# Kernel tuning notes

Measured on AMD Instinct MI355X. Metric: run time of the kernel, lower is better.

Reference implementation:

```python
import jax, jax.numpy as jnp
import numpy as np

N_NODES = 100_000
N_EDGES = 3_200_000
N_FEAT = 128
N_HID = 8
N_CLASSES = 10


def setup_inputs() -> dict:
    key = jax.random.key(0)
    ks = jax.random.split(key, 16)
    g = lambda k, shape, fan_in: jax.random.normal(k, shape, jnp.float32) / np.sqrt(fan_in)
    inp = {}
    inp['x'] = jax.random.normal(ks[0], (N_NODES, N_FEAT), jnp.float32)
    inp['edge_index'] = jax.random.randint(ks[1], (2, N_EDGES), 0, N_NODES, jnp.int32)
    # lin: Linear(F, 8)
    inp['lin_w'] = g(ks[2], (N_FEAT, N_HID), N_FEAT)
    inp['lin_b'] = jnp.zeros((N_HID,), jnp.float32)
    # conv1: GATConv(8, 8, heads=2)
    inp['w1'] = g(ks[3], (N_HID, 2 * N_HID), N_HID)
    inp['a1_src'] = g(ks[4], (2, N_HID), N_HID)
    inp['a1_dst'] = g(ks[5], (2, N_HID), N_HID)
    inp['b1'] = jnp.zeros((2 * N_HID,), jnp.float32)
    # conv2: GATConv(16, 8, heads=2)
    inp['w2'] = g(ks[6], (2 * N_HID, 2 * N_HID), 2 * N_HID)
    inp['a2_src'] = g(ks[7], (2, N_HID), N_HID)
    inp['a2_dst'] = g(ks[8], (2, N_HID), N_HID)
    inp['b2'] = jnp.zeros((2 * N_HID,), jnp.float32)
    # conv3: GATConv(16, num_classes, heads=1, concat=False)
    inp['w3'] = g(ks[9], (2 * N_HID, N_CLASSES), 2 * N_HID)
    inp['a3_src'] = g(ks[10], (1, N_CLASSES), N_CLASSES)
    inp['a3_dst'] = g(ks[11], (1, N_CLASSES), N_CLASSES)
    inp['b3'] = jnp.zeros((N_CLASSES,), jnp.float32)
    return inp


def _gat_conv(x, W, a_src, a_dst, b, src, dst, heads, out_c, concat):
    """PyG GATConv with pre-appended self-loops in (src, dst)."""
    N = x.shape[0]
    xl = (x @ W).reshape(N, heads, out_c)                 # [N,H,C]
    alpha_src = (xl * a_src[None]).sum(-1)                # [N,H]
    alpha_dst = (xl * a_dst[None]).sum(-1)                # [N,H]
    e = jax.nn.leaky_relu(alpha_src[src] + alpha_dst[dst], 0.2)  # [E,H]
    # segment softmax over destination nodes
    m = jax.ops.segment_max(e, dst, num_segments=N)
    e = jnp.exp(e - m[dst])
    s = jax.ops.segment_sum(e, dst, num_segments=N)
    alpha = e / s[dst]                                    # [E,H]
    msg = xl[src] * alpha[:, :, None]                     # [E,H,C]
    out = jax.ops.segment_sum(msg, dst, num_segments=N)   # [N,H,C]
    out = out.reshape(N, heads * out_c) if concat else out.mean(axis=1)
    return out + b


def reference(x, edge_index, lin_w, lin_b, w1, a1_src, a1_dst, b1,
              w2, a2_src, a2_dst, b2, w3, a3_src, a3_dst, b3):
    N = x.shape[0]
    loops = jnp.arange(N, dtype=edge_index.dtype)
    src = jnp.concatenate([edge_index[0], loops])
    dst = jnp.concatenate([edge_index[1], loops])
    lrelu = lambda v: jax.nn.leaky_relu(v, 0.01)
    h = lrelu(x @ lin_w + lin_b)
    h = lrelu(_gat_conv(h, w1, a1_src, a1_dst, b1, src, dst, 2, N_HID, True))
    h = lrelu(_gat_conv(h, w2, a2_src, a2_dst, b2, src, dst, 2, N_HID, True))
    h = _gat_conv(h, w3, a3_src, a3_dst, b3, src, dst, 1, N_CLASSES, False)
    return jax.nn.log_softmax(h, axis=-1)
```

## Files before the change

### kernel.cpp

```cpp
#include <hip/hip_runtime.h>
#include <hip/hip_fp16.h>
#include <math.h>

#define N_NODES 100000
#define N_EDGES 3200000
#define ET (N_EDGES + N_NODES)
#define SLOT 80
#define KMAX 5
#define SHIFT 8
#define BNODES 256
#define NBUCK 391
#define BCAP 9088
#define P1_T 1024
#define E_PER 16
#define P1_WG ((N_EDGES + P1_T * E_PER - 1) / (P1_T * E_PER))
#define SCAN_T 1024
#define SCAN_CHUNK 98
#define LOG2E 1.44269504088896f

__device__ __forceinline__ float lrelu(float v, float s) { return v > 0.f ? v : v * s; }
__device__ __forceinline__ float fexp2(float x) { return __builtin_amdgcn_exp2f(x); }

template <int CTRL>
__device__ __forceinline__ float dppmov(float v) {
    return __int_as_float(__builtin_amdgcn_update_dpp(0, __float_as_int(v), CTRL, 0xF, 0xF, true));
}

__device__ __forceinline__ void reduce16(float& v, float& ssum, float pa0, float pa1,
                                         float pa2, float pa3, int lane) {
    int b0 = lane & 1, b1 = (lane >> 1) & 1;
    float k0 = b0 ? pa2 : pa0, g0 = b0 ? pa0 : pa2;
    float k1 = b0 ? pa3 : pa1, g1 = b0 ? pa1 : pa3;
    float q0 = k0 + dppmov<0xB1>(g0);
    float q1 = k1 + dppmov<0xB1>(g1);
    float kk = b1 ? q1 : q0, gg = b1 ? q0 : q1;
    v = kk + dppmov<0x4E>(gg);
    v += __shfl_xor(v, 4, 64);
    v += __shfl_xor(v, 8, 64);
    ssum += dppmov<0xB1>(ssum);
    ssum += dppmov<0x4E>(ssum);
    ssum += __shfl_xor(ssum, 4, 64);
    ssum += __shfl_xor(ssum, 8, 64);
}

__global__ void __launch_bounds__(P1_T) part_kernel(const int* __restrict__ ei,
                                                    int* __restrict__ bcur,
                                                    unsigned* __restrict__ pairs) {
    __shared__ int hist[NBUCK];
    __shared__ int gbase[NBUCK];
    int t = threadIdx.x;
    for (int i = t; i < NBUCK; i += P1_T) hist[i] = 0;
    __syncthreads();
    int base = blockIdx.x * (P1_T * E_PER);
    int s[E_PER], d[E_PER], r[E_PER];
#pragma unroll
    for (int k = 0; k < E_PER; k++) {
        int e = base + k * P1_T + t;
        if (e < N_EDGES) {
            s[k] = ei[e];
            d[k] = ei[N_EDGES + e];
            r[k] = atomicAdd(&hist[d[k] >> SHIFT], 1);
        }
    }
    __syncthreads();
    for (int i = t; i < NBUCK; i += P1_T)
        gbase[i] = (hist[i] > 0) ? atomicAdd(&bcur[i], hist[i]) : 0;
    __syncthreads();
#pragma unroll
    for (int k = 0; k < E_PER; k++) {
        int e = base + k * P1_T + t;
        if (e < N_EDGES) {
            int b = d[k] >> SHIFT;
            int pos = gbase[b] + r[k];
            if (pos < BCAP)
                pairs[(size_t)b * BCAP + pos] =
                    ((unsigned)(d[k] & (BNODES - 1)) << 17) | (unsigned)s[k];
        }
    }
}

__global__ void build_kernel(const int* __restrict__ bcur, const unsigned* __restrict__ pairs,
                             int* __restrict__ csr, int* __restrict__ deg) {
    __shared__ int offs[BNODES];
    int b = blockIdx.x;
    int t = threadIdx.x;
    int node0 = b << SHIFT;
    int n = node0 + t;
    if (n < N_NODES) {
        csr[n * SLOT] = n;
        offs[t] = 1;
    } else offs[t] = 0;
    __syncthreads();
    int cnt = min(bcur[b], BCAP);
    for (int i = t; i < cnt; i += BNODES) {
        unsigned v = pairs[(size_t)b * BCAP + i];
        int ln = v >> 17;
        int s = v & 0x1FFFF;
        int pos = atomicAdd(&offs[ln], 1);
        if (pos < SLOT) csr[(node0 + ln) * SLOT + pos] = s;
    }
    __syncthreads();
    if (n < N_NODES) deg[n] = offs[t];
}

__global__ void count_kernel(const int* __restrict__ ei, int* __restrict__ deg) {
    int e = blockIdx.x * blockDim.x + threadIdx.x;
    if (e >= ET) return;
    int d = (e < N_EDGES) ? ei[N_EDGES + e] : (e - N_EDGES);
    atomicAdd(&deg[d], 1);
}

__global__ void scan_kernel(const int* __restrict__ deg, int* __restrict__ rowptr,
                            int* __restrict__ cursor) {
    __shared__ int sums[SCAN_T];
    int t = threadIdx.x;
    int start = t * SCAN_CHUNK;
    int end = min(start + SCAN_CHUNK, N_NODES);
    int s = 0;
    for (int i = start; i < end; i++) s += deg[i];
    sums[t] = s;
    __syncthreads();
    for (int off = 1; off < SCAN_T; off <<= 1) {
        int v = sums[t];
        int add = (t >= off) ? sums[t - off] : 0;
        __syncthreads();
        sums[t] = v + add;
        __syncthreads();
    }
    int base = (t > 0) ? sums[t - 1] : 0;
    for (int i = start; i < end; i++) {
        rowptr[i] = base;
        cursor[i] = base;
        base += deg[i];
    }
    if (t == SCAN_T - 1) rowptr[N_NODES] = base;
}

__global__ void scatter_kernel(const int* __restrict__ ei, int* __restrict__ cursor,
                               int* __restrict__ csr) {
    int e = blockIdx.x * blockDim.x + threadIdx.x;
    if (e >= ET) return;
    int s, d;
    if (e < N_EDGES) { s = ei[e]; d = ei[N_EDGES + e]; } else { s = d = e - N_EDGES; }
    int pos = atomicAdd(&cursor[d], 1);
    csr[pos] = s;
}

template <int CIN, int H, int C, int XLS>
__global__ void prep_kernel(const float* __restrict__ hin, const float* __restrict__ W,
                            const float* __restrict__ a_src, const float* __restrict__ a_dst,
                            __half* __restrict__ xl, float* __restrict__ asrc,
                            float* __restrict__ adst) {
    __shared__ float Ws[CIN * H * C];
    __shared__ float As[H * C];
    __shared__ float Ad[H * C];
    for (int i = threadIdx.x; i < CIN * H * C; i += blockDim.x) Ws[i] = W[i];
    for (int i = threadIdx.x; i < H * C; i += blockDim.x) {
        As[i] = a_src[i] * LOG2E;
        Ad[i] = a_dst[i] * LOG2E;
    }
    __syncthreads();
    int n = blockIdx.x * blockDim.x + threadIdx.x;
    if (n >= N_NODES) return;
    float hreg[CIN];
#pragma unroll
    for (int i = 0; i < CIN; i += 4) {
        float4 v = *(const float4*)&hin[n * CIN + i];
        hreg[i] = v.x; hreg[i + 1] = v.y; hreg[i + 2] = v.z; hreg[i + 3] = v.w;
    }
#pragma unroll
    for (int h = 0; h < H; h++) {
        float as = 0.f, ad = 0.f;
#pragma unroll
        for (int c = 0; c < C; c++) {
            float v = 0.f;
#pragma unroll
            for (int i = 0; i < CIN; i++) v += hreg[i] * Ws[i * H * C + h * C + c];
            xl[n * XLS + h * C + c] = __float2half_rn(v);
            as += v * As[h * C + c];
            ad += v * Ad[h * C + c];
        }
        asrc[n * H + h] = as;
        adst[n * H + h] = ad;
    }
#pragma unroll
    for (int c = H * C; c < XLS; c++) xl[n * XLS + c] = __float2half_rn(0.f);
}

template <int H, int C, int XLS>
__global__ __launch_bounds__(256) void prep_lin_kernel(
        const float* __restrict__ x, const float* __restrict__ lw, const float* __restrict__ lb,
        const float* __restrict__ W, const float* __restrict__ a_src,
        const float* __restrict__ a_dst, __half* __restrict__ xl,
        float* __restrict__ asrc, float* __restrict__ adst) {
    __shared__ float LW[128 * 8];
    __shared__ float Ws[8 * H * C];
    __shared__ float As[H * C];
    __shared__ float Ad[H * C];
    __shared__ float Lb[8];
    for (int i = threadIdx.x; i < 128 * 8; i += 256) LW[i] = lw[i];
    for (int i = threadIdx.x; i < 8 * H * C; i += 256) Ws[i] = W[i];
    for (int i = threadIdx.x; i < H * C; i += 256) {
        As[i] = a_src[i] * LOG2E;
        Ad[i] = a_dst[i] * LOG2E;
    }
    if (threadIdx.x < 8) Lb[threadIdx.x] = lb[threadIdx.x];
    __syncthreads();
    int n = blockIdx.x * blockDim.x + threadIdx.x;
    if (n >= N_NODES) return;
    float hreg[8];
#pragma unroll
    for (int c = 0; c < 8; c++) hreg[c] = 0.f;
#pragma unroll 8
    for (int i = 0; i < 128; i += 4) {
        float4 v = *(const float4*)&x[n * 128 + i];
#pragma unroll
        for (int c = 0; c < 8; c++) hreg[c] += v.x * LW[(i + 0) * 8 + c];
#pragma unroll
        for (int c = 0; c < 8; c++) hreg[c] += v.y * LW[(i + 1) * 8 + c];
#pragma unroll
        for (int c = 0; c < 8; c++) hreg[c] += v.z * LW[(i + 2) * 8 + c];
#pragma unroll
        for (int c = 0; c < 8; c++) hreg[c] += v.w * LW[(i + 3) * 8 + c];
    }
#pragma unroll
    for (int c = 0; c < 8; c++) hreg[c] = lrelu(hreg[c] + Lb[c], 0.01f);
#pragma unroll
    for (int h = 0; h < H; h++) {
        float as = 0.f, ad = 0.f;
#pragma unroll
        for (int c = 0; c < C; c++) {
            float v = 0.f;
#pragma unroll
            for (int i = 0; i < 8; i++) v += hreg[i] * Ws[i * H * C + h * C + c];
            xl[n * XLS + h * C + c] = __float2half_rn(v);
            as += v * As[h * C + c];
            ad += v * Ad[h * C + c];
        }
        asrc[n * H + h] = as;
        adst[n * H + h] = ad;
    }
#pragma unroll
    for (int c = H * C; c < XLS; c++) xl[n * XLS + c] = __float2half_rn(0.f);
}

__global__ __launch_bounds__(256) void gat64_h2(const int* __restrict__ cnt_,
                                                const int* __restrict__ csr,
                                                const float* __restrict__ asrc,
                                                const float* __restrict__ adst,
                                                const __half* __restrict__ xl,
                                                const float* __restrict__ b,
                                                float* __restrict__ hout) {
    int wg = blockIdx.x * 4 + (threadIdx.x >> 6);
    int lane = threadIdx.x & 63;
    int eg = lane & 15;
    int cp = lane >> 4;
    int h = cp >> 1;
    int n0 = wg * 2, n1 = n0 + 1;
    int cnt0 = min(cnt_[n0], SLOT);
    int cnt1 = min(cnt_[n1], SLOT);
    int ka0 = __builtin_amdgcn_readfirstlane((cnt0 + 15) >> 4);
    int ka1 = __builtin_amdgcn_readfirstlane((cnt1 + 15) >> 4);
    float ad0 = adst[n0 * 2 + h];
    float ad1 = adst[n1 * 2 + h];
    int idx0[KMAX], idx1[KMAX];
#pragma unroll
    for (int k = 0; k < KMAX; k++) {
        if (k < ka0) idx0[k] = csr[n0 * SLOT + eg + (k << 4)];
        if (k < ka1) idx1[k] = csr[n1 * SLOT + eg + (k << 4)];
    }
    float s0 = 0.f, a00 = 0.f, a01 = 0.f, a02 = 0.f, a03 = 0.f;
    float s1 = 0.f, a10 = 0.f, a11 = 0.f, a12 = 0.f, a13 = 0.f;
#pragma unroll
    for (int k = 0; k < KMAX; k++) {
        if (k < ka0) {
            bool vld = eg + (k << 4) < cnt0;
            int s = vld ? idx0[k] : 0;
            float av = asrc[s * 2 + h];
            float2 raw = *(const float2*)&xl[s * 16 + 4 * cp];
            float e = av + ad0;
            float w = fexp2(fmaxf(e, 0.2f * e));
            w = vld ? w : 0.f;
            float2 f01 = __half22float2(*(__half2*)&raw.x);
            float2 f23 = __half22float2(*(__half2*)&raw.y);
            s0 += w;
            a00 += w * f01.x; a01 += w * f01.y; a02 += w * f23.x; a03 += w * f23.y;
        }
        if (k < ka1) {
            bool vld = eg + (k << 4) < cnt1;
            int t = vld ? idx1[k] : 0;
            float av = asrc[t * 2 + h];
            float2 raw = *(const float2*)&xl[t * 16 + 4 * cp];
            float e = av + ad1;
            float w = fexp2(fmaxf(e, 0.2f * e));
            w = vld ? w : 0.f;
            float2 f01 = __half22float2(*(__half2*)&raw.x);
            float2 f23 = __half22float2(*(__half2*)&raw.y);
            s1 += w;
            a10 += w * f01.x; a11 += w * f01.y; a12 += w * f23.x; a13 += w * f23.y;
        }
    }
    float v0, v1;
    reduce16(v0, s0, a00, a01, a02, a03, lane);
    reduce16(v1, s1, a10, a11, a12, a13, lane);
    if ((lane & 12) == 0) {
        int ch = 4 * cp + 2 * (lane & 1) + ((lane >> 1) & 1);
        float bc = b[ch];
        hout[n0 * 16 + ch] = lrelu(v0 / s0 + bc, 0.01f);
        hout[n1 * 16 + ch] = lrelu(v1 / s1 + bc, 0.01f);
    }
}

__global__ __launch_bounds__(256) void gat64_ls(const int* __restrict__ cnt_,
                                                const int* __restrict__ csr,
                                                const float* __restrict__ asrc,
                                                const float* __restrict__ adst,
                                                const __half* __restrict__ xl,
                                                const float* __restrict__ b,
                                                float* __restrict__ out) {
    int wg = blockIdx.x * 4 + (threadIdx.x >> 6);
    int lane = threadIdx.x & 63;
    int eg = lane & 15;
    int cp = lane >> 4;
    int n0 = wg * 2, n1 = n0 + 1;
    int cnt0 = min(cnt_[n0], SLOT);
    int cnt1 = min(cnt_[n1], SLOT);
    int ka0 = __builtin_amdgcn_readfirstlane((cnt0 + 15) >> 4);
    int ka1 = __builtin_amdgcn_readfirstlane((cnt1 + 15) >> 4);
    float ad0 = adst[n0];
    float ad1 = adst[n1];
    int idx0[KMAX], idx1[KMAX];
#pragma unroll
    for (int k = 0; k < KMAX; k++) {
        if (k < ka0) idx0[k] = csr[n0 * SLOT + eg + (k << 4)];
        if (k < ka1) idx1[k] = csr[n1 * SLOT + eg + (k << 4)];
    }
    float s0 = 0.f, a00 = 0.f, a01 = 0.f, a02 = 0.f, a03 = 0.f;
    float s1 = 0.f, a10 = 0.f, a11 = 0.f, a12 = 0.f, a13 = 0.f;
#pragma unroll
    for (int k = 0; k < KMAX; k++) {
        if (k < ka0) {
            bool vld = eg + (k << 4) < cnt0;
            int s = vld ? idx0[k] : 0;
            float av = asrc[s];
            float2 raw = *(const float2*)&xl[s * 16 + 4 * cp];
            float e = av + ad0;
            float w = fexp2(fmaxf(e, 0.2f * e));
            w = vld ? w : 0.f;
            float2 f01 = __half22float2(*(__half2*)&raw.x);
            float2 f23 = __half22float2(*(__half2*)&raw.y);
            s0 += w;
            a00 += w * f01.x; a01 += w * f01.y; a02 += w * f23.x; a03 += w * f23.y;
        }
        if (k < ka1) {
            bool vld = eg + (k << 4) < cnt1;
            int t = vld ? idx1[k] : 0;
            float av = asrc[t];
            float2 raw = *(const float2*)&xl[t * 16 + 4 * cp];
            float e = av + ad1;
            float w = fexp2(fmaxf(e, 0.2f * e));
            w = vld ? w : 0.f;
            float2 f01 = __half22float2(*(__half2*)&raw.x);
            float2 f23 = __half22float2(*(__half2*)&raw.y);
            s1 += w;
            a10 += w * f01.x; a11 += w * f01.y; a12 += w * f23.x; a13 += w * f23.y;
        }
    }
    float v0, v1;
    reduce16(v0, s0, a00, a01, a02, a03, lane);
    reduce16(v1, s1, a10, a11, a12, a13, lane);
    int ch = 4 * cp + 2 * (lane & 1) + ((lane >> 1) & 1);
    float bc = (ch < 10) ? b[ch] : 0.f;
    float u0 = (ch < 10) ? v0 / s0 + bc : -INFINITY;
    float u1 = (ch < 10) ? v1 / s1 + bc : -INFINITY;
    float m0 = u0, m1 = u1;
    m0 = fmaxf(m0, dppmov<0xB1>(m0)); m1 = fmaxf(m1, dppmov<0xB1>(m1));
    m0 = fmaxf(m0, dppmov<0x4E>(m0)); m1 = fmaxf(m1, dppmov<0x4E>(m1));
    m0 = fmaxf(m0, __shfl_xor(m0, 16, 64)); m1 = fmaxf(m1, __shfl_xor(m1, 16, 64));
    m0 = fmaxf(m0, __shfl_xor(m0, 32, 64)); m1 = fmaxf(m1, __shfl_xor(m1, 32, 64));
    float e0 = (ch < 10) ? __expf(u0 - m0) : 0.f;
    float e1 = (ch < 10) ? __expf(u1 - m1) : 0.f;
    e0 += dppmov<0xB1>(e0); e1 += dppmov<0xB1>(e1);
    e0 += dppmov<0x4E>(e0); e1 += dppmov<0x4E>(e1);
    e0 += __shfl_xor(e0, 16, 64); e1 += __shfl_xor(e1, 16, 64);
    e0 += __shfl_xor(e0, 32, 64); e1 += __shfl_xor(e1, 32, 64);
    float lse0 = m0 + __logf(e0);
    float lse1 = m1 + __logf(e1);
    if ((lane & 12) == 0 && ch < 10) {
        out[n0 * 10 + ch] = u0 - lse0;
        out[n1 * 10 + ch] = u1 - lse1;
    }
}

__global__ void gat16_h2(const int* __restrict__ rowptr, const int* __restrict__ csr,
                         const float* __restrict__ asrc, const float* __restrict__ adst,
                         const __half* __restrict__ xl, const float* __restrict__ b,
                         float* __restrict__ hout) {
    int tid = blockIdx.x * blockDim.x + threadIdx.x;
    int wave = tid >> 6;
    int lane = threadIdx.x & 63;
    int g = lane >> 4;
    int c = lane & 15;
    int h = c >> 3;
    int n = wave * 4 + g;
    if (n >= N_NODES) return;
    int beg = rowptr[n], cnt = rowptr[n + 1] - beg;
    float adn = adst[n * 2 + h];
    float ssum = 0.f, pa = 0.f;
#pragma unroll 4
    for (int i = 0; i < cnt; i++) {
        int s = csr[beg + i];
        float e = asrc[s * 2 + h] + adn;
        float w = fexp2(fmaxf(e, 0.2f * e));
        ssum += w;
        pa += w * __half2float(xl[s * 16 + c]);
    }
    hout[n * 16 + c] = lrelu(pa / ssum + b[c], 0.01f);
}

__global__ void gat16_ls(const int* __restrict__ rowptr, const int* __restrict__ csr,
                         const float* __restrict__ asrc, const float* __restrict__ adst,
                         const __half* __restrict__ xl, const float* __restrict__ b,
                         float* __restrict__ out) {
    int tid = blockIdx.x * blockDim.x + threadIdx.x;
    int wave = tid >> 6;
    int lane = threadIdx.x & 63;
    int g = lane >> 4;
    int c = lane & 15;
    int n = wave * 4 + g;
    if (n >= N_NODES) return;
    int beg = rowptr[n], cnt = rowptr[n + 1] - beg;
    float adn = adst[n];
    float ssum = 0.f, pa = 0.f;
#pragma unroll 4
    for (int i = 0; i < cnt; i++) {
        int s = csr[beg + i];
        float e = asrc[s] + adn;
        float w = fexp2(fmaxf(e, 0.2f * e));
        ssum += w;
        pa += w * __half2float(xl[s * 16 + c]);
    }
    float v = pa / ssum + ((c < 10) ? b[c] : 0.f);
    float vm = (c < 10) ? v : -INFINITY;
#pragma unroll
    for (int off = 8; off >= 1; off >>= 1) vm = fmaxf(vm, __shfl_xor(vm, off, 16));
    float ex = (c < 10) ? __expf(v - vm) : 0.f;
    float sum = ex;
#pragma unroll
    for (int off = 8; off >= 1; off >>= 1) sum += __shfl_xor(sum, off, 16);
    float lse = vm + __logf(sum);
    if (c < 10) out[n * 10 + c] = v - lse;
}

extern "C" void kernel_launch(void* const* d_in, const int* in_sizes, int n_in,
                              void* d_out, int out_size, void* d_ws, size_t ws_size,
                              hipStream_t stream) {
    const float* x     = (const float*)d_in[0];
    const int*   ei    = (const int*)d_in[1];
    const float* lin_w = (const float*)d_in[2];
    const float* lin_b = (const float*)d_in[3];
    const float* w1    = (const float*)d_in[4];
    const float* a1s   = (const float*)d_in[5];
    const float* a1d   = (const float*)d_in[6];
    const float* b1    = (const float*)d_in[7];
    const float* w2    = (const float*)d_in[8];
    const float* a2s   = (const float*)d_in[9];
    const float* a2d   = (const float*)d_in[10];
    const float* b2    = (const float*)d_in[11];
    const float* w3    = (const float*)d_in[12];
    const float* a3s   = (const float*)d_in[13];
    const float* a3d   = (const float*)d_in[14];
    const float* b3    = (const float*)d_in[15];

    float* ws = (float*)d_ws;
    float* slotH  = ws;
    __half* slotX = (__half*)(ws + 1600000);
    float* as_    = ws + 3200000;
    float* ad_    = ws + 3400000;
    unsigned* pairs = (unsigned*)ws;
    int* csrP = (int*)(ws + 3600000);
    int* degP = (int*)(ws + 3600000 + N_NODES * SLOT);
    int* bcur = degP + N_NODES;
    size_t need_new = (size_t)(3600000 + N_NODES * SLOT + N_NODES + 512) * 4;

    int use_bucket = (ws_size >= need_new) ? 1 : 0;

    int* degC    = (int*)(ws + 3600000);
    int* rowptrC = degC + N_NODES;
    int* cursorC = rowptrC + N_NODES + 1;
    int* csrC    = cursorC + N_NODES;

    dim3 B(256);
    int nb_n  = (N_NODES + 255) / 256;
    int nb_et = (ET + 255) / 256;
    int nb_g  = (N_NODES + 15) / 16;
    int nb_w2 = N_NODES / 8;

    if (use_bucket) {
        hipMemsetAsync(bcur, 0, 512 * sizeof(int), stream);
        part_kernel<<<P1_WG, P1_T, 0, stream>>>(ei, bcur, pairs);
        build_kernel<<<NBUCK, BNODES, 0, stream>>>(bcur, pairs, csrP, degP);
    } else {
        hipMemsetAsync(degC, 0, N_NODES * sizeof(int), stream);
        count_kernel<<<nb_et, B, 0, stream>>>(ei, degC);
        scan_kernel<<<1, SCAN_T, 0, stream>>>(degC, rowptrC, cursorC);
        scatter_kernel<<<nb_et, B, 0, stream>>>(ei, cursorC, csrC);
    }

    prep_lin_kernel<2, 8, 16><<<nb_n, B, 0, stream>>>(x, lin_w, lin_b, w1, a1s, a1d,
                                                      slotX, as_, ad_);
    if (use_bucket) gat64_h2<<<nb_w2, B, 0, stream>>>(degP, csrP, as_, ad_, slotX, b1, slotH);
    else            gat16_h2<<<nb_g, B, 0, stream>>>(rowptrC, csrC, as_, ad_, slotX, b1, slotH);

    prep_kernel<16, 2, 8, 16><<<nb_n, B, 0, stream>>>(slotH, w2, a2s, a2d, slotX, as_, ad_);
    if (use_bucket) gat64_h2<<<nb_w2, B, 0, stream>>>(degP, csrP, as_, ad_, slotX, b2, slotH);
    else            gat16_h2<<<nb_g, B, 0, stream>>>(rowptrC, csrC, as_, ad_, slotX, b2, slotH);

    prep_kernel<16, 1, 10, 16><<<nb_n, B, 0, stream>>>(slotH, w3, a3s, a3d, slotX, as_, ad_);
    if (use_bucket) gat64_ls<<<nb_w2, B, 0, stream>>>(degP, csrP, as_, ad_, slotX, b3, (float*)d_out);
    else            gat16_ls<<<nb_g, B, 0, stream>>>(rowptrC, csrC, as_, ad_, slotX, b3, (float*)d_out);
}
```

Before: 328.9 us.

## Recompute source attention scores from gathered fp16 features via dot2 instead of gathering asrc

The aggregation kernels no longer gather the precomputed per-node source attention logit. Each lane instead recomputes it from the fp16 feature row it already loads, using packed fp16 dot-product instructions against the attention vector. The lane mapping also changes: each half-wave now handles one node with 8 channels per lane and 16-byte loads, in place of two interleaved nodes with 4 channels per lane. This removes one random gather per edge, at the cost of extra ALU work and reduced precision in the attention logits, since the attention vector is rounded to fp16.

```diff
diff --git a/kernel.cpp b/kernel.cpp
--- a/kernel.cpp
+++ b/kernel.cpp
@@ -18,25 +18,39 @@
 #define SCAN_CHUNK 98
 #define LOG2E 1.44269504088896f
 
+typedef _Float16 h2 __attribute__((ext_vector_type(2)));
+
 __device__ __forceinline__ float lrelu(float v, float s) { return v > 0.f ? v : v * s; }
 __device__ __forceinline__ float fexp2(float x) { return __builtin_amdgcn_exp2f(x); }
+
+__device__ __forceinline__ h2 f2h2(float f) {
+    union { float f; h2 h; } u; u.f = f; return u.h;
+}
+
+__device__ __forceinline__ float fdot2(h2 a, h2 b, float c) {
+#if __has_builtin(__builtin_amdgcn_fdot2)
+    return __builtin_amdgcn_fdot2(a, b, c, false);
+#else
+    return c + (float)a.x * (float)b.x + (float)a.y * (float)b.y;
+#endif
+}
 
 template <int CTRL>
 __device__ __forceinline__ float dppmov(float v) {
     return __int_as_float(__builtin_amdgcn_update_dpp(0, __float_as_int(v), CTRL, 0xF, 0xF, true));
 }
 
-__device__ __forceinline__ void reduce16(float& v, float& ssum, float pa0, float pa1,
-                                         float pa2, float pa3, int lane) {
-    int b0 = lane & 1, b1 = (lane >> 1) & 1;
-    float k0 = b0 ? pa2 : pa0, g0 = b0 ? pa0 : pa2;
-    float k1 = b0 ? pa3 : pa1, g1 = b0 ? pa1 : pa3;
-    float q0 = k0 + dppmov<0xB1>(g0);
-    float q1 = k1 + dppmov<0xB1>(g1);
-    float kk = b1 ? q1 : q0, gg = b1 ? q0 : q1;
-    v = kk + dppmov<0x4E>(gg);
-    v += __shfl_xor(v, 4, 64);
-    v += __shfl_xor(v, 8, 64);
+__device__ __forceinline__ void reduce8(float a[8], float& ssum, int lane) {
+    int b0 = lane & 1, b1 = (lane >> 1) & 1, b2 = (lane >> 2) & 1;
+    float q0 = (b0 ? a[4] : a[0]) + dppmov<0xB1>(b0 ? a[0] : a[4]);
+    float q1 = (b0 ? a[5] : a[1]) + dppmov<0xB1>(b0 ? a[1] : a[5]);
+    float q2 = (b0 ? a[6] : a[2]) + dppmov<0xB1>(b0 ? a[2] : a[6]);
+    float q3 = (b0 ? a[7] : a[3]) + dppmov<0xB1>(b0 ? a[3] : a[7]);
+    float r0 = (b1 ? q2 : q0) + dppmov<0x4E>(b1 ? q0 : q2);
+    float r1 = (b1 ? q3 : q1) + dppmov<0x4E>(b1 ? q1 : q3);
+    float t  = (b2 ? r1 : r0) + __shfl_xor(b2 ? r0 : r1, 4, 64);
+    t += __shfl_xor(t, 8, 64);
+    a[0] = t;
     ssum += dppmov<0xB1>(ssum);
     ssum += dppmov<0x4E>(ssum);
     ssum += __shfl_xor(ssum, 4, 64);
@@ -246,7 +260,7 @@
 
 __global__ __launch_bounds__(256) void gat64_h2(const int* __restrict__ cnt_,
                                                 const int* __restrict__ csr,
-                                                const float* __restrict__ asrc,
+                                                const float* __restrict__ a_src,
                                                 const float* __restrict__ adst,
                                                 const __half* __restrict__ xl,
                                                 const float* __restrict__ b,
@@ -254,66 +268,50 @@
     int wg = blockIdx.x * 4 + (threadIdx.x >> 6);
     int lane = threadIdx.x & 63;
     int eg = lane & 15;
-    int cp = lane >> 4;
-    int h = cp >> 1;
-    int n0 = wg * 2, n1 = n0 + 1;
-    int cnt0 = min(cnt_[n0], SLOT);
-    int cnt1 = min(cnt_[n1], SLOT);
-    int ka0 = __builtin_amdgcn_readfirstlane((cnt0 + 15) >> 4);
-    int ka1 = __builtin_amdgcn_readfirstlane((cnt1 + 15) >> 4);
-    float ad0 = adst[n0 * 2 + h];
-    float ad1 = adst[n1 * 2 + h];
-    int idx0[KMAX], idx1[KMAX];
+    int q  = (lane >> 4) & 1;
+    int nd = lane >> 5;
+    int n = wg * 2 + nd;
+    float4 as0 = *(const float4*)&a_src[q * 8];
+    float4 as1 = *(const float4*)&a_src[q * 8 + 4];
+    h2 av0 = {(_Float16)(as0.x * LOG2E), (_Float16)(as0.y * LOG2E)};
+    h2 av1 = {(_Float16)(as0.z * LOG2E), (_Float16)(as0.w * LOG2E)};
+    h2 av2 = {(_Float16)(as1.x * LOG2E), (_Float16)(as1.y * LOG2E)};
+    h2 av3 = {(_Float16)(as1.z * LOG2E), (_Float16)(as1.w * LOG2E)};
+    int cnt = min(cnt_[n], SLOT);
+    float ad = adst[n * 2 + q];
+    int idx[KMAX];
 #pragma unroll
     for (int k = 0; k < KMAX; k++) {
-        if (k < ka0) idx0[k] = csr[n0 * SLOT + eg + (k << 4)];
-        if (k < ka1) idx1[k] = csr[n1 * SLOT + eg + (k << 4)];
-    }
-    float s0 = 0.f, a00 = 0.f, a01 = 0.f, a02 = 0.f, a03 = 0.f;
-    float s1 = 0.f, a10 = 0.f, a11 = 0.f, a12 = 0.f, a13 = 0.f;
+        int i = eg + (k << 4);
+        idx[k] = (i < cnt) ? csr[n * SLOT + i] : -1;
+    }
+    float ssum = 0.f;
+    float a[8] = {0.f, 0.f, 0.f, 0.f, 0.f, 0.f, 0.f, 0.f};
 #pragma unroll
     for (int k = 0; k < KMAX; k++) {
-        if (k < ka0) {
-            bool vld = eg + (k << 4) < cnt0;
-            int s = vld ? idx0[k] : 0;
-            float av = asrc[s * 2 + h];
-            float2 raw = *(const float2*)&xl[s * 16 + 4 * cp];
-            float e = av + ad0;
+        int s = idx[k];
+        if (s >= 0) {
+            float4 raw = *(const float4*)&xl[s * 16 + q * 8];
+            h2 x0 = f2h2(raw.x), x1 = f2h2(raw.y), x2 = f2h2(raw.z), x3 = f2h2(raw.w);
+            float e = fdot2(x0, av0, fdot2(x1, av1, fdot2(x2, av2, fdot2(x3, av3, ad))));
             float w = fexp2(fmaxf(e, 0.2f * e));
-            w = vld ? w : 0.f;
-            float2 f01 = __half22float2(*(__half2*)&raw.x);
-            float2 f23 = __half22float2(*(__half2*)&raw.y);
-            s0 += w;
-            a00 += w * f01.x; a01 += w * f01.y; a02 += w * f23.x; a03 += w * f23.y;
+            ssum += w;
+            a[0] += w * (float)x0.x; a[1] += w * (float)x0.y;
+            a[2] += w * (float)x1.x; a[3] += w * (float)x1.y;
+            a[4] += w * (float)x2.x; a[5] += w * (float)x2.y;
+            a[6] += w * (float)x3.x; a[7] += w * (float)x3.y;
         }
-        if (k < ka1) {
-            bool vld = eg + (k << 4) < cnt1;
-            int t = vld ? idx1[k] : 0;
-            float av = asrc[t * 2 + h];
-            float2 raw = *(const float2*)&xl[t * 16 + 4 * cp];
-            float e = av + ad1;
-            float w = fexp2(fmaxf(e, 0.2f * e));
-            w = vld ? w : 0.f;
-            float2 f01 = __half22float2(*(__half2*)&raw.x);
-            float2 f23 = __half22float2(*(__half2*)&raw.y);
-            s1 += w;
-            a10 += w * f01.x; a11 += w * f01.y; a12 += w * f23.x; a13 += w * f23.y;
-        }
-    }
-    float v0, v1;
-    reduce16(v0, s0, a00, a01, a02, a03, lane);
-    reduce16(v1, s1, a10, a11, a12, a13, lane);
-    if ((lane & 12) == 0) {
-        int ch = 4 * cp + 2 * (lane & 1) + ((lane >> 1) & 1);
-        float bc = b[ch];
-        hout[n0 * 16 + ch] = lrelu(v0 / s0 + bc, 0.01f);
-        hout[n1 * 16 + ch] = lrelu(v1 / s1 + bc, 0.01f);
+    }
+    reduce8(a, ssum, lane);
+    if ((lane & 8) == 0) {
+        int ch = 8 * q + 4 * (lane & 1) + 2 * ((lane >> 1) & 1) + ((lane >> 2) & 1);
+        hout[n * 16 + ch] = lrelu(a[0] / ssum + b[ch], 0.01f);
     }
 }
 
 __global__ __launch_bounds__(256) void gat64_ls(const int* __restrict__ cnt_,
                                                 const int* __restrict__ csr,
-                                                const float* __restrict__ asrc,
+                                                const float* __restrict__ a_src,
                                                 const float* __restrict__ adst,
                                                 const __half* __restrict__ xl,
                                                 const float* __restrict__ b,
@@ -321,75 +319,62 @@
     int wg = blockIdx.x * 4 + (threadIdx.x >> 6);
     int lane = threadIdx.x & 63;
     int eg = lane & 15;
-    int cp = lane >> 4;
-    int n0 = wg * 2, n1 = n0 + 1;
-    int cnt0 = min(cnt_[n0], SLOT);
-    int cnt1 = min(cnt_[n1], SLOT);
-    int ka0 = __builtin_amdgcn_readfirstlane((cnt0 + 15) >> 4);
-    int ka1 = __builtin_amdgcn_readfirstlane((cnt1 + 15) >> 4);
-    float ad0 = adst[n0];
-    float ad1 = adst[n1];
-    int idx0[KMAX], idx1[KMAX];
+    int q  = (lane >> 4) & 1;
+    int nd = lane >> 5;
+    int n = wg * 2 + nd;
+    float avf[8];
+#pragma unroll
+    for (int j = 0; j < 8; j++) {
+        int c = q * 8 + j;
+        avf[j] = (c < 10) ? a_src[c] * LOG2E : 0.f;
+    }
+    h2 av0 = {(_Float16)avf[0], (_Float16)avf[1]};
+    h2 av1 = {(_Float16)avf[2], (_Float16)avf[3]};
+    h2 av2 = {(_Float16)avf[4], (_Float16)avf[5]};
+    h2 av3 = {(_Float16)avf[6], (_Float16)avf[7]};
+    int cnt = min(cnt_[n], SLOT);
+    float adh = adst[n] * 0.5f;
+    int idx[KMAX];
 #pragma unroll
     for (int k = 0; k < KMAX; k++) {
-        if (k < ka0) idx0[k] = csr[n0 * SLOT + eg + (k << 4)];
-        if (k < ka1) idx1[k] = csr[n1 * SLOT + eg + (k << 4)];
-    }
-    float s0 = 0.f, a00 = 0.f, a01 = 0.f, a02 = 0.f, a03 = 0.f;
-    float s1 = 0.f, a10 = 0.f, a11 = 0.f, a12 = 0.f, a13 = 0.f;
+        int i = eg + (k << 4);
+        idx[k] = (i < cnt) ? csr[n * SLOT + i] : -1;
+    }
+    float ssum = 0.f;
+    float a[8] = {0.f, 0.f, 0.f, 0.f, 0.f, 0.f, 0.f, 0.f};
 #pragma unroll
     for (int k = 0; k < KMAX; k++) {
-        if (k < ka0) {
-            bool vld = eg + (k << 4) < cnt0;
-            int s = vld ? idx0[k] : 0;
-            float av = asrc[s];
-            float2 raw = *(const float2*)&xl[s * 16 + 4 * cp];
-            float e = av + ad0;
+        int s = idx[k];
+        if (s >= 0) {
+            float4 raw = *(const float4*)&xl[s * 16 + q * 8];
+            h2 x0 = f2h2(raw.x), x1 = f2h2(raw.y), x2 = f2h2(raw.z), x3 = f2h2(raw.w);
+            float part = fdot2(x0, av0, fdot2(x1, av1, fdot2(x2, av2, fdot2(x3, av3, adh))));
+            float e = part + __shfl_xor(part, 16, 64);
             float w = fexp2(fmaxf(e, 0.2f * e));
-            w = vld ? w : 0.f;
-            float2 f01 = __half22float2(*(__half2*)&raw.x);
-            float2 f23 = __half22float2(*(__half2*)&raw.y);
-            s0 += w;
-            a00 += w * f01.x; a01 += w * f01.y; a02 += w * f23.x; a03 += w * f23.y;
+            ssum += w;
+            a[0] += w * (float)x0.x; a[1] += w * (float)x0.y;
+            a[2] += w * (float)x1.x; a[3] += w * (float)x1.y;
+            a[4] += w * (float)x2.x; a[5] += w * (float)x2.y;
+            a[6] += w * (float)x3.x; a[7] += w * (float)x3.y;
         }
-        if (k < ka1) {
-            bool vld = eg + (k << 4) < cnt1;
-            int t = vld ? idx1[k] : 0;
-            float av = asrc[t];
-            float2 raw = *(const float2*)&xl[t * 16 + 4 * cp];
-            float e = av + ad1;
-            float w = fexp2(fmaxf(e, 0.2f * e));
-            w = vld ? w : 0.f;
-            float2 f01 = __half22float2(*(__half2*)&raw.x);
-            float2 f23 = __half22float2(*(__half2*)&raw.y);
-            s1 += w;
-            a10 += w * f01.x; a11 += w * f01.y; a12 += w * f23.x; a13 += w * f23.y;
-        }
-    }
-    float v0, v1;
-    reduce16(v0, s0, a00, a01, a02, a03, lane);
-    reduce16(v1, s1, a10, a11, a12, a13, lane);
-    int ch = 4 * cp + 2 * (lane & 1) + ((lane >> 1) & 1);
-    float bc = (ch < 10) ? b[ch] : 0.f;
-    float u0 = (ch < 10) ? v0 / s0 + bc : -INFINITY;
-    float u1 = (ch < 10) ? v1 / s1 + bc : -INFINITY;
-    float m0 = u0, m1 = u1;
-    m0 = fmaxf(m0, dppmov<0xB1>(m0)); m1 = fmaxf(m1, dppmov<0xB1>(m1));
-    m0 = fmaxf(m0, dppmov<0x4E>(m0)); m1 = fmaxf(m1, dppmov<0x4E>(m1));
-    m0 = fmaxf(m0, __shfl_xor(m0, 16, 64)); m1 = fmaxf(m1, __shfl_xor(m1, 16, 64));
-    m0 = fmaxf(m0, __shfl_xor(m0, 32, 64)); m1 = fmaxf(m1, __shfl_xor(m1, 32, 64));
-    float e0 = (ch < 10) ? __expf(u0 - m0) : 0.f;
-    float e1 = (ch < 10) ? __expf(u1 - m1) : 0.f;
-    e0 += dppmov<0xB1>(e0); e1 += dppmov<0xB1>(e1);
-    e0 += dppmov<0x4E>(e0); e1 += dppmov<0x4E>(e1);
-    e0 += __shfl_xor(e0, 16, 64); e1 += __shfl_xor(e1, 16, 64);
-    e0 += __shfl_xor(e0, 32, 64); e1 += __shfl_xor(e1, 32, 64);
-    float lse0 = m0 + __logf(e0);
-    float lse1 = m1 + __logf(e1);
-    if ((lane & 12) == 0 && ch < 10) {
-        out[n0 * 10 + ch] = u0 - lse0;
-        out[n1 * 10 + ch] = u1 - lse1;
-    }
+    }
+    reduce8(a, ssum, lane);
+    int ch = 8 * q + 4 * (lane & 1) + 2 * ((lane >> 1) & 1) + ((lane >> 2) & 1);
+    float u = (ch < 10) ? a[0] / ssum + b[ch] : -INFINITY;
+    float m = u;
+    m = fmaxf(m, dppmov<0xB1>(m));
+    m = fmaxf(m, dppmov<0x4E>(m));
+    m = fmaxf(m, __shfl_xor(m, 4, 64));
+    m = fmaxf(m, __shfl_xor(m, 8, 64));
+    m = fmaxf(m, __shfl_xor(m, 16, 64));
+    float ex = (ch < 10 && (lane & 8) == 0) ? __expf(u - m) : 0.f;
+    ex += dppmov<0xB1>(ex);
+    ex += dppmov<0x4E>(ex);
+    ex += __shfl_xor(ex, 4, 64);
+    ex += __shfl_xor(ex, 8, 64);
+    ex += __shfl_xor(ex, 16, 64);
+    float lse = m + __logf(ex);
+    if ((lane & 8) == 0 && ch < 10) out[n * 10 + ch] = u - lse;
 }
 
 __global__ void gat16_h2(const int* __restrict__ rowptr, const int* __restrict__ csr,
@@ -509,14 +494,14 @@
 
     prep_lin_kernel<2, 8, 16><<<nb_n, B, 0, stream>>>(x, lin_w, lin_b, w1, a1s, a1d,
                                                       slotX, as_, ad_);
-    if (use_bucket) gat64_h2<<<nb_w2, B, 0, stream>>>(degP, csrP, as_, ad_, slotX, b1, slotH);
+    if (use_bucket) gat64_h2<<<nb_w2, B, 0, stream>>>(degP, csrP, a1s, ad_, slotX, b1, slotH);
     else            gat16_h2<<<nb_g, B, 0, stream>>>(rowptrC, csrC, as_, ad_, slotX, b1, slotH);
 
     prep_kernel<16, 2, 8, 16><<<nb_n, B, 0, stream>>>(slotH, w2, a2s, a2d, slotX, as_, ad_);
-    if (use_bucket) gat64_h2<<<nb_w2, B, 0, stream>>>(degP, csrP, as_, ad_, slotX, b2, slotH);
+    if (use_bucket) gat64_h2<<<nb_w2, B, 0, stream>>>(degP, csrP, a2s, ad_, slotX, b2, slotH);
     else            gat16_h2<<<nb_g, B, 0, stream>>>(rowptrC, csrC, as_, ad_, slotX, b2, slotH);
 
     prep_kernel<16, 1, 10, 16><<<nb_n, B, 0, stream>>>(slotH, w3, a3s, a3d, slotX, as_, ad_);
-    if (use_bucket) gat64_ls<<<nb_w2, B, 0, stream>>>(degP, csrP, as_, ad_, slotX, b3, (float*)d_out);
+    if (use_bucket) gat64_ls<<<nb_w2, B, 0, stream>>>(degP, csrP, a3s, ad_, slotX, b3, (float*)d_out);
     else            gat16_ls<<<nb_g, B, 0, stream>>>(rowptrC, csrC, as_, ad_, slotX, b3, (float*)d_out);
 }
```

Result: faster. 280.9 us (-14.6%).
